# Kernel tuning notes

Hardware: AMD Instinct MI355X
Metric: run time of the kernel (lower is better)

The kernel has to match this reference:

```python
import jax, jax.numpy as jnp
import numpy as np

N_NODES = 50000  # 4 node types x 12500
N_PER = 12500
E = 600000
H = 128
IN_DIMS = [128, 128, 64, 64]


def setup_inputs() -> dict:
    key = jax.random.key(0)
    ks = jax.random.split(key, 16)
    inp = {}
    for i, d in enumerate(IN_DIMS):
        inp[f"feat{i}"] = jax.random.normal(ks[i], (N_PER, d), dtype=jnp.float32)
        # xavier_normal-ish init, gain 1.414
        std = 1.414 * np.sqrt(2.0 / (d + H))
        inp[f"W_fc{i}"] = jax.random.normal(ks[4 + i], (d, H), dtype=jnp.float32) * std
        inp[f"b_fc{i}"] = jnp.zeros((H,), dtype=jnp.float32)
    inp["src"] = jax.random.randint(ks[8], (E,), 0, N_NODES, dtype=jnp.int32)
    inp["dst"] = jax.random.randint(ks[9], (E,), 0, N_NODES, dtype=jnp.int32)
    inp["e_feat"] = jax.random.randint(ks[10], (E,), 0, 36, dtype=jnp.int32)
    inp["b_g0"] = jnp.zeros((H,), dtype=jnp.float32)  # GraphConv layer0 (weight=False, bias)
    inp["W_g1"] = jax.random.normal(ks[11], (H, H), dtype=jnp.float32) * np.sqrt(1.0 / H)
    inp["b_g1"] = jnp.zeros((H,), dtype=jnp.float32)
    return inp


def _degree_norms(src, dst):
    ones = jnp.ones((src.shape[0],), dtype=jnp.float32)
    deg_out = jax.ops.segment_sum(ones, src, num_segments=N_NODES)
    deg_in = jax.ops.segment_sum(ones, dst, num_segments=N_NODES)
    # DGL norm='both': D_out^{-1/2} on src side, D_in^{-1/2} on dst side (clamp 0-degree)
    out_norm = jax.lax.rsqrt(jnp.maximum(deg_out, 1.0))
    in_norm = jax.lax.rsqrt(jnp.maximum(deg_in, 1.0))
    return out_norm, in_norm


def _gcn_aggregate(h, src, dst, out_norm, in_norm):
    m = (h * out_norm[:, None])[src]                      # [E, H] gather
    agg = jax.ops.segment_sum(m, dst, num_segments=N_NODES)
    return agg * in_norm[:, None]


def reference(feat0, feat1, feat2, feat3,
              W_fc0, b_fc0, W_fc1, b_fc1, W_fc2, b_fc2, W_fc3, b_fc3,
              src, dst, e_feat, b_g0, W_g1, b_g1):
    # per-node-type linear projections, then concat along node dim
    h = jnp.concatenate([
        feat0 @ W_fc0 + b_fc0,
        feat1 @ W_fc1 + b_fc1,
        feat2 @ W_fc2 + b_fc2,
        feat3 @ W_fc3 + b_fc3,
    ], axis=0)  # [N_NODES, H]

    out_norm, in_norm = _degree_norms(src, dst)
    # GraphConv layer 0: weight=False, bias, activation (dropout p=0 -> identity)
    h = jax.nn.relu(_gcn_aggregate(h, src, dst, out_norm, in_norm) + b_g0)
    # GraphConv layer 1: aggregate, then linear weight + bias, activation
    h = jax.nn.relu(_gcn_aggregate(h, src, dst, out_norm, in_norm) @ W_g1 + b_g1)

    e = e_feat.astype(jnp.float32)  # e_feat.reshape(-1,1).float() in original
    # forward graph: msg = ft + sum_{r in 0..4} where(e==r, ft, 0) = ft * (1 + 1{e in 0..4})
    w_fwd = 1.0 + sum((e == float(r)).astype(jnp.float32) for r in (0, 1, 2, 3, 4))
    agg_a = jax.ops.segment_sum(h[src] * w_fwd[:, None], dst, num_segments=N_NODES)
    # transpose graph (reversed edges, same e): msg = sum_{r in {6,14,30}} where(e==r, ft, 0)
    w_bwd = sum((e == float(r)).astype(jnp.float32) for r in (6, 14, 30))
    agg_b = jax.ops.segment_sum(h[dst] * w_bwd[:, None], src, num_segments=N_NODES)
    return agg_a + agg_b
```

## Files before the change

### kernel.cpp

```cpp
#include <hip/hip_runtime.h>
#include <hip/hip_bf16.h>

#define N_NODES 50000
#define N_PER   12500
#define E_EDGES 600000
#define HDIM    128

#define NBLK_FC    ((N_PER + 63) / 64)
#define NBLK_NODE  ((N_NODES + 255) / 256)
#define MASK31  0x7fffffff

#define HQD 64
#define HSL_D (E_EDGES / HQD)
#define NBLK_DB (HQD * 4)

typedef __attribute__((ext_vector_type(8))) short bfrag;
typedef __attribute__((ext_vector_type(4))) float ffrag;

__device__ __forceinline__ unsigned short f2bf(float f) {
    union { float f; unsigned u; } x; x.f = f;
    unsigned r = x.u + 0x7fffu + ((x.u >> 16) & 1u);
    return (unsigned short)(r >> 16);
}
__device__ __forceinline__ float lo_bf(unsigned v) { return __uint_as_float(v << 16); }
__device__ __forceinline__ float hi_bf(unsigned v) { return __uint_as_float(v & 0xffff0000u); }
__device__ __forceinline__ unsigned pack2(float a, float b) {
    return (unsigned)f2bf(a) | ((unsigned)f2bf(b) << 16);
}
__device__ __forceinline__ float onrm_of(int deg) {
    return rsqrtf(fmaxf((float)deg, 1.0f));
}

__device__ __forceinline__ void acc8_add(float* acc, uint4 v) {
    acc[0] += lo_bf(v.x); acc[1] += hi_bf(v.x);
    acc[2] += lo_bf(v.y); acc[3] += hi_bf(v.y);
    acc[4] += lo_bf(v.z); acc[5] += hi_bf(v.z);
    acc[6] += lo_bf(v.w); acc[7] += hi_bf(v.w);
}
__device__ __forceinline__ void acc8_addw(float* acc, uint4 v, float w) {
    acc[0] += lo_bf(v.x) * w; acc[1] += hi_bf(v.x) * w;
    acc[2] += lo_bf(v.y) * w; acc[3] += hi_bf(v.y) * w;
    acc[4] += lo_bf(v.z) * w; acc[5] += hi_bf(v.z) * w;
    acc[6] += lo_bf(v.w) * w; acc[7] += hi_bf(v.w) * w;
}

__global__ __launch_bounds__(1024) void prep_kernel(
    const float* __restrict__ W0, const float* __restrict__ W1,
    const float* __restrict__ W2, const float* __restrict__ W3,
    const float* __restrict__ Wg,
    const int* __restrict__ src, const int* __restrict__ dst,
    const int* __restrict__ ef,
    unsigned short* __restrict__ Wp,
    unsigned* __restrict__ partial) {
    __shared__ unsigned hist[N_PER];
    int b = blockIdx.x;
    if (b < NBLK_DB) {
        const int q = b >> 2;
        const int p = b & 3;
        const int g0 = p * N_PER;
        for (int j = threadIdx.x; j < N_PER; j += 1024) hist[j] = 0;
        __syncthreads();
        const int e0 = q * HSL_D;
        for (int i = e0 + threadIdx.x; i < e0 + HSL_D; i += 1024) {
            int d = dst[i], t = ef[i], s = src[i];
            unsigned rd = (unsigned)(d - g0);
            if (rd < (unsigned)N_PER) atomicAdd(&hist[rd], 1u);
            unsigned rs = (unsigned)(s - g0);
            if (rs < (unsigned)N_PER) {
                unsigned inc = 0x10000u
                             + ((t == 6 || t == 14 || t == 30) ? 0x400u : 0u);
                atomicAdd(&hist[rs], inc);
            }
        }
        __syncthreads();
        for (int j = threadIdx.x; j < N_PER; j += 1024)
            partial[(size_t)q * N_NODES + g0 + j] = hist[j];
    } else {
        int tid = (b - NBLK_DB) * 1024 + threadIdx.x;
        const float* W; int D, base, off;
        if      (tid < 2048) { W = W0; D = 128; base = 0;    off = 0;     }
        else if (tid < 4096) { W = W1; D = 128; base = 2048; off = 16384; }
        else if (tid < 5120) { W = W2; D = 64;  base = 4096; off = 32768; }
        else if (tid < 6144) { W = W3; D = 64;  base = 5120; off = 40960; }
        else                 { W = Wg; D = 128; base = 6144; off = 49152; }
        int t2 = tid - base;
        int KT = D / 32;
        int l = t2 & 63;
        int tt = t2 >> 6;
        int kt = tt % KT, n0 = tt / KT;
        int n = n0 * 16 + (l & 15);
        int kb = kt * 32 + (l >> 4) * 8;
#pragma unroll
        for (int j = 0; j < 8; ++j)
            Wp[(size_t)off + (size_t)t2 * 8 + j] = f2bf(W[(size_t)(kb + j) * 128 + n]);
    }
}

__global__ __launch_bounds__(256) void plane_prefix_kernel(
    unsigned* __restrict__ partial,
    int* __restrict__ degD, int* __restrict__ degB,
    int* __restrict__ scanD, int* __restrict__ scanB,
    int* __restrict__ blocksumD, int* __restrict__ blocksumB,
    float* __restrict__ onrm_buf) {
    const int t = threadIdx.x;
    const int n = blockIdx.x * 256 + t;
    int dA = 0, dD = 0, dB = 0;
    if (n < N_NODES) {
        int runD = 0, runB = 0, dS = 0;
#pragma unroll
        for (int q = 0; q < HQD; ++q) {
            size_t ix = (size_t)q * N_NODES + n;
            unsigned w = partial[ix];
            partial[ix] = (unsigned)runD | ((unsigned)runB << 10);
            runD += (int)(w & 0x3FFu);
            runB += (int)((w >> 10) & 0x3Fu);
            dS   += (int)(w >> 16);
        }
        dD = runD; dB = runB;
        degD[n] = dD; degB[n] = dB;
        onrm_buf[n] = onrm_of(dS);
        dA = (dD + 3) & ~3;
    }
    __shared__ int sD[256], sB[256];
    sD[t] = dA; sB[t] = dB;
    __syncthreads();
    for (int off = 1; off < 256; off <<= 1) {
        int xD = (t >= off) ? sD[t - off] : 0;
        int xB = (t >= off) ? sB[t - off] : 0;
        __syncthreads();
        sD[t] += xD; sB[t] += xB;
        __syncthreads();
    }
    if (n < N_NODES) {
        scanD[n] = sD[t] - dA;
        scanB[n] = sB[t] - dB;
    }
    if (t == 255) {
        blocksumD[blockIdx.x] = sD[255];
        blocksumB[blockIdx.x] = sB[255];
    }
}

__global__ __launch_bounds__(256) void base_add_kernel(
    const int* __restrict__ blocksumD, const int* __restrict__ blocksumB,
    const int* __restrict__ scanD, const int* __restrict__ scanB,
    const int* __restrict__ degD, const int* __restrict__ degB,
    int2* __restrict__ csrD, int2* __restrict__ csrB) {
    __shared__ int sD[256], sB[256];
    const int t = threadIdx.x;
    const int bid = blockIdx.x;
    sD[t] = (t < bid) ? blocksumD[t] : 0;
    sB[t] = (t < bid) ? blocksumB[t] : 0;
    __syncthreads();
    for (int off = 128; off >= 1; off >>= 1) {
        if (t < off) { sD[t] += sD[t + off]; sB[t] += sB[t + off]; }
        __syncthreads();
    }
    const int n = bid * 256 + t;
    if (n < N_NODES) {
        csrD[n] = make_int2(scanD[n] + sD[0], degD[n]);
        csrB[n] = make_int2(scanB[n] + sB[0], degB[n]);
    }
}

template<int D>
__device__ __forceinline__ void fc_body(
    int blk, int tid,
    const float* __restrict__ X,
    const unsigned short* __restrict__ Wp,
    const float* __restrict__ bias,
    const float* __restrict__ onrm,
    unsigned short* __restrict__ outbf,
    int rows)
{
    constexpr int KT = D / 32;
    const int lane = tid & 63;
    const int wave = tid >> 6;
    const int m = lane & 15, q = lane >> 4;
    const int rbase = blk * 64 + wave * 16;
    const int row = rbase + m;

    bfrag afr[KT];
#pragma unroll
    for (int kt = 0; kt < KT; ++kt) {
        bfrag a;
        if (row < rows) {
            const float* xp = X + (size_t)row * D + kt * 32 + q * 8;
            float4 u0 = *(const float4*)xp;
            float4 u1 = *(const float4*)(xp + 4);
            a[0] = (short)f2bf(u0.x); a[1] = (short)f2bf(u0.y);
            a[2] = (short)f2bf(u0.z); a[3] = (short)f2bf(u0.w);
            a[4] = (short)f2bf(u1.x); a[5] = (short)f2bf(u1.y);
            a[6] = (short)f2bf(u1.z); a[7] = (short)f2bf(u1.w);
        } else {
#pragma unroll
            for (int t = 0; t < 8; ++t) a[t] = 0;
        }
        afr[kt] = a;
    }

    ffrag acc[8];
#pragma unroll
    for (int n0 = 0; n0 < 8; ++n0)
#pragma unroll
        for (int t = 0; t < 4; ++t) acc[n0][t] = 0.f;

#pragma unroll
    for (int n0 = 0; n0 < 8; ++n0)
#pragma unroll
        for (int kt = 0; kt < KT; ++kt) {
            bfrag bfr = *(const bfrag*)(Wp + ((size_t)(n0 * KT + kt) * 64 + lane) * 8);
            acc[n0] = __builtin_amdgcn_mfma_f32_16x16x32_bf16(afr[kt], bfr, acc[n0], 0, 0, 0);
        }

#pragma unroll
    for (int n0 = 0; n0 < 8; ++n0) {
        const int col = n0 * 16 + m;
        const float bj = bias[col];
#pragma unroll
        for (int r = 0; r < 4; ++r) {
            int orow = rbase + q * 4 + r;
            if (orow < rows)
                outbf[(size_t)orow * 128 + col] =
                    f2bf((acc[n0][r] + bj) * onrm[orow]);
        }
    }
}

__global__ __launch_bounds__(1024) void scatfc_kernel(
    const int* __restrict__ src, const int* __restrict__ dst,
    const int* __restrict__ ef,
    const unsigned* __restrict__ partial,
    const int2* __restrict__ csrD, const int2* __restrict__ csrB,
    int* __restrict__ bucket, int* __restrict__ bucketB,
    const float* __restrict__ f0, const float* __restrict__ f1,
    const float* __restrict__ f2, const float* __restrict__ f3,
    const unsigned short* __restrict__ Wp,
    const float* __restrict__ b0, const float* __restrict__ b1,
    const float* __restrict__ b2, const float* __restrict__ b3,
    const float* __restrict__ onrm_buf,
    unsigned short* __restrict__ Abf)
{
    __shared__ unsigned offP[N_PER];
    const int b = blockIdx.x;
    if (b < NBLK_DB) {
        const int q = b >> 2;
        const int p = b & 3;
        const int g0 = p * N_PER;
        for (int j = threadIdx.x; j < N_PER; j += 1024) {
            unsigned w = partial[(size_t)q * N_NODES + g0 + j];
            offP[j] = (unsigned)(csrD[g0 + j].x + (int)(w & 0x3FFu))
                    | (((w >> 10) & 0x3Fu) << 20);
        }
        __syncthreads();
        const int e0 = q * HSL_D;
        for (int i = e0 + threadIdx.x; i < e0 + HSL_D; i += 1024) {
            int s = src[i], d = dst[i], t = ef[i];
            unsigned rd = (unsigned)(d - g0);
            if (rd < (unsigned)N_PER) {
                unsigned old = atomicAdd(&offP[rd], 1u);
                bucket[old & 0xFFFFFu] = s | ((t <= 4) ? 0x80000000 : 0);
            }
            if (t == 6 || t == 14 || t == 30) {
                unsigned rs = (unsigned)(s - g0);
                if (rs < (unsigned)N_PER) {
                    unsigned old = atomicAdd(&offP[rs], 1u << 20);
                    bucketB[csrB[s].x + (int)(old >> 20)] = d;
                }
            }
        }
    } else {
        int ft = (b - NBLK_DB) * 4 + (threadIdx.x >> 8);
        int tid = threadIdx.x & 255;
        int which = ft / NBLK_FC;
        int blk = ft - which * NBLK_FC;
        if (which == 0)
            fc_body<128>(blk, tid, f0, Wp,         b0, onrm_buf,
                         Abf + (size_t)0 * N_PER * HDIM, N_PER);
        else if (which == 1)
            fc_body<128>(blk, tid, f1, Wp + 16384, b1, onrm_buf + N_PER,
                         Abf + (size_t)1 * N_PER * HDIM, N_PER);
        else if (which == 2)
            fc_body<64>(blk, tid, f2, Wp + 32768, b2, onrm_buf + 2 * N_PER,
                        Abf + (size_t)2 * N_PER * HDIM, N_PER);
        else
            fc_body<64>(blk, tid, f3, Wp + 40960, b3, onrm_buf + 3 * N_PER,
                        Abf + (size_t)3 * N_PER * HDIM, N_PER);
    }
}

#define GATHER8(DSTARR)                                                       \
    for (; i + 8 <= cnt; i += 8) {                                            \
        int4 c0 = *(const int4*)(bk + i);                                     \
        int4 c1 = *(const int4*)(bk + i + 4);                                 \
        int cc[8] = {c0.x, c0.y, c0.z, c0.w, c1.x, c1.y, c1.z, c1.w};         \
        uint4 v[8];                                                           \
        _Pragma("unroll")                                                     \
        for (int k = 0; k < 8; ++k)                                           \
            v[k] = DSTARR[(size_t)(cc[k] & MASK31) * 16 + j8];                \
        _Pragma("unroll")                                                     \
        for (int k = 0; k < 8; ++k) acc8_add(acc, v[k]);                      \
    }                                                                         \
    if (i + 4 <= cnt) {                                                       \
        int4 c0 = *(const int4*)(bk + i);                                     \
        int cc[4] = {c0.x, c0.y, c0.z, c0.w};                                 \
        uint4 v[4];                                                           \
        _Pragma("unroll")                                                     \
        for (int k = 0; k < 4; ++k)                                           \
            v[k] = DSTARR[(size_t)(cc[k] & MASK31) * 16 + j8];                \
        _Pragma("unroll")                                                     \
        for (int k = 0; k < 4; ++k) acc8_add(acc, v[k]);                      \
        i += 4;                                                               \
    }                                                                         \
    for (; i < cnt; ++i)                                                      \
        acc8_add(acc, DSTARR[(size_t)(bk[i] & MASK31) * 16 + j8]);

__global__ __launch_bounds__(256) void agg0g_kernel(
    const uint4* __restrict__ A,
    const int* __restrict__ bucket, const int2* __restrict__ csrD,
    const float* __restrict__ onrm_buf, const float* __restrict__ b_g0,
    const unsigned short* __restrict__ Wp,
    unsigned short* __restrict__ BW) {
    __shared__ uint4 Bt[256];
    const int tdx = threadIdx.x;
    const int nloc = tdx >> 4, j8 = tdx & 15;
    const int n = blockIdx.x * 16 + nloc;

    const int2 cd = csrD[n];
    const int cnt = cd.y;
    const int* bk = bucket + cd.x;
    float acc[8] = {0.f, 0.f, 0.f, 0.f, 0.f, 0.f, 0.f, 0.f};
    int i = 0;
    GATHER8(A)

    float inr = onrm_of(cnt);
    float onr = onrm_buf[n];
    const float* bg = b_g0 + j8 * 8;
    float r[8];
#pragma unroll
    for (int k = 0; k < 8; ++k)
        r[k] = fmaxf(acc[k] * inr + bg[k], 0.f) * onr;
    uint4 o;
    o.x = pack2(r[0], r[1]); o.y = pack2(r[2], r[3]);
    o.z = pack2(r[4], r[5]); o.w = pack2(r[6], r[7]);
    Bt[j8 * 16 + nloc] = o;
    __syncthreads();

    const int lane = tdx & 63;
    const int wave = tdx >> 6;
    const int m = lane & 15, q = lane >> 4;

    bfrag afr[4];
#pragma unroll
    for (int kt = 0; kt < 4; ++kt)
        afr[kt] = *(const bfrag*)(Bt + (kt * 4 + q) * 16 + m);

    ffrag acc2[2];
#pragma unroll
    for (int t2 = 0; t2 < 2; ++t2) {
#pragma unroll
        for (int t = 0; t < 4; ++t) acc2[t2][t] = 0.f;
        const int n0 = wave * 2 + t2;
#pragma unroll
        for (int kt = 0; kt < 4; ++kt) {
            bfrag bfr = *(const bfrag*)(Wp + ((size_t)(n0 * 4 + kt) * 64 + lane) * 8);
            acc2[t2] = __builtin_amdgcn_mfma_f32_16x16x32_bf16(afr[kt], bfr, acc2[t2], 0, 0, 0);
        }
    }

    const int rowbase = blockIdx.x * 16;
#pragma unroll
    for (int t2 = 0; t2 < 2; ++t2) {
        const int col = (wave * 2 + t2) * 16 + m;
#pragma unroll
        for (int rr = 0; rr < 4; ++rr) {
            const int row = rowbase + q * 4 + rr;
            BW[(size_t)row * 128 + col] = f2bf(acc2[t2][rr]);
        }
    }
}

__global__ __launch_bounds__(256) void agg1_kernel(
    const uint4* __restrict__ BW,
    const int* __restrict__ bucket, const int2* __restrict__ csrD,
    const float* __restrict__ b_g1,
    uint4* __restrict__ H) {
    int idx = blockIdx.x * blockDim.x + threadIdx.x;
    int n = idx >> 4, j8 = idx & 15;
    const int2 cd = csrD[n];
    const int cnt = cd.y;
    const int* bk = bucket + cd.x;
    float acc[8] = {0.f, 0.f, 0.f, 0.f, 0.f, 0.f, 0.f, 0.f};
    int i = 0;
    GATHER8(BW)
    float inr = onrm_of(cnt);
    const float* bg = b_g1 + j8 * 8;
    float r[8];
#pragma unroll
    for (int k = 0; k < 8; ++k)
        r[k] = fmaxf(acc[k] * inr + bg[k], 0.f);
    uint4 o;
    o.x = pack2(r[0], r[1]); o.y = pack2(r[2], r[3]);
    o.z = pack2(r[4], r[5]); o.w = pack2(r[6], r[7]);
    H[(size_t)n * 16 + j8] = o;
}

__global__ __launch_bounds__(256) void final_kernel(
    const uint4* __restrict__ H,
    const int* __restrict__ bucket, const int2* __restrict__ csrD,
    const int* __restrict__ bucketB, const int2* __restrict__ csrB,
    float4* __restrict__ out4) {
    int idx = blockIdx.x * blockDim.x + threadIdx.x;
    int n = idx >> 4, j8 = idx & 15;
    float acc[8] = {0.f, 0.f, 0.f, 0.f, 0.f, 0.f, 0.f, 0.f};
    const int2 cd = csrD[n];
    const int cnt = cd.y;
    const int* bk = bucket + cd.x;
    int i = 0;
    for (; i + 8 <= cnt; i += 8) {
        int4 c0 = *(const int4*)(bk + i);
        int4 c1 = *(const int4*)(bk + i + 4);
        int cc[8] = {c0.x, c0.y, c0.z, c0.w, c1.x, c1.y, c1.z, c1.w};
        uint4 v[8];
#pragma unroll
        for (int k = 0; k < 8; ++k)
            v[k] = H[(size_t)(cc[k] & MASK31) * 16 + j8];
#pragma unroll
        for (int k = 0; k < 8; ++k)
            acc8_addw(acc, v[k], (cc[k] < 0) ? 2.0f : 1.0f);
    }
    if (i + 4 <= cnt) {
        int4 c0 = *(const int4*)(bk + i);
        int cc[4] = {c0.x, c0.y, c0.z, c0.w};
        uint4 v[4];
#pragma unroll
        for (int k = 0; k < 4; ++k)
            v[k] = H[(size_t)(cc[k] & MASK31) * 16 + j8];
#pragma unroll
        for (int k = 0; k < 4; ++k)
            acc8_addw(acc, v[k], (cc[k] < 0) ? 2.0f : 1.0f);
        i += 4;
    }
    for (; i < cnt; ++i) {
        int c = bk[i];
        acc8_addw(acc, H[(size_t)(c & MASK31) * 16 + j8], (c < 0) ? 2.0f : 1.0f);
    }
    const int2 cb = csrB[n];
    const int* bkB = bucketB + cb.x;
    for (int k = 0; k < cb.y; ++k)
        acc8_add(acc, H[(size_t)bkB[k] * 16 + j8]);
    float4 o0 = {acc[0], acc[1], acc[2], acc[3]};
    float4 o1 = {acc[4], acc[5], acc[6], acc[7]};
    out4[(size_t)n * 32 + j8 * 2]     = o0;
    out4[(size_t)n * 32 + j8 * 2 + 1] = o1;
}

extern "C" void kernel_launch(void* const* d_in, const int* in_sizes, int n_in,
                              void* d_out, int out_size, void* d_ws, size_t ws_size,
                              hipStream_t stream) {
    const float* feat[4]  = {(const float*)d_in[0], (const float*)d_in[3],
                             (const float*)d_in[6], (const float*)d_in[9]};
    const float* W_fc[4]  = {(const float*)d_in[1], (const float*)d_in[4],
                             (const float*)d_in[7], (const float*)d_in[10]};
    const float* b_fc[4]  = {(const float*)d_in[2], (const float*)d_in[5],
                             (const float*)d_in[8], (const float*)d_in[11]};
    const int*   src      = (const int*)d_in[12];
    const int*   dst      = (const int*)d_in[13];
    const int*   efeat    = (const int*)d_in[14];
    const float* b_g0     = (const float*)d_in[15];
    const float* W_g1     = (const float*)d_in[16];
    const float* b_g1     = (const float*)d_in[17];
    float* out = (float*)d_out;

    char* p = (char*)d_ws;
    unsigned short* Abf = (unsigned short*)p; p += (size_t)N_NODES * HDIM * 2;
    unsigned short* Bbf = (unsigned short*)p; p += (size_t)N_NODES * HDIM * 2;
    unsigned short* Wp  = (unsigned short*)p; p += (size_t)65536 * 2;
    int* bucket  = (int*)p; p += (size_t)(E_EDGES + 4 * N_NODES) * 4;
    int* bucketB = (int*)p; p += (size_t)E_EDGES * 4;
    unsigned* partial = (unsigned*)p; p += (size_t)HQD * N_NODES * 4;
    int* degD  = (int*)p; p += (size_t)N_NODES * 4;
    int* degB  = (int*)p; p += (size_t)N_NODES * 4;
    int* scanD = (int*)p; p += (size_t)N_NODES * 4;
    int* scanB = (int*)p; p += (size_t)N_NODES * 4;
    int2* csrD = (int2*)p; p += (size_t)N_NODES * 8;
    int2* csrB = (int2*)p; p += (size_t)N_NODES * 8;
    float* onrm_buf = (float*)p; p += (size_t)N_NODES * 4;
    int* blocksumD = (int*)p; p += 256 * 4;
    int* blocksumB = (int*)p; p += 256 * 4;

    const unsigned short* Wpg = Wp + 49152;

    prep_kernel<<<NBLK_DB + 8, 1024, 0, stream>>>(
        W_fc[0], W_fc[1], W_fc[2], W_fc[3], W_g1, src, dst, efeat,
        Wp, partial);

    plane_prefix_kernel<<<NBLK_NODE, 256, 0, stream>>>(
        partial, degD, degB, scanD, scanB, blocksumD, blocksumB, onrm_buf);

    base_add_kernel<<<NBLK_NODE, 256, 0, stream>>>(
        blocksumD, blocksumB, scanD, scanB, degD, degB, csrD, csrB);

    scatfc_kernel<<<NBLK_DB + NBLK_FC, 1024, 0, stream>>>(
        src, dst, efeat, partial, csrD, csrB, bucket, bucketB,
        feat[0], feat[1], feat[2], feat[3], Wp,
        b_fc[0], b_fc[1], b_fc[2], b_fc[3], onrm_buf, Abf);

    const int grid_node = (N_NODES * 16) / 256;

    agg0g_kernel<<<grid_node, 256, 0, stream>>>(
        (const uint4*)Abf, bucket, csrD, onrm_buf, b_g0, Wpg, Bbf);

    agg1_kernel<<<grid_node, 256, 0, stream>>>(
        (const uint4*)Bbf, bucket, csrD, b_g1, (uint4*)Abf);

    final_kernel<<<grid_node, 256, 0, stream>>>(
        (const uint4*)Abf, bucket, csrD, bucketB, csrB, (float4*)out);
}
```

Baseline: 226.2 us.

## Sort nodes by in-degree into a permutation to balance aggregation waves

Builds a degree histogram (bins 0..63) per block during the prefix pass, then computes a global counting-sort permutation of nodes by in-degree in the base-add kernel. The three aggregation kernels iterate over nodes through this permutation, so nodes with similar edge counts share a wave and divergence from uneven loop trip counts shrinks. The cost is an extra indirection per node, scattered output writes instead of contiguous ones, and some extra histogram work in the setup kernels. Reads from the feature array may also lose some locality.

```diff
diff --git a/kernel.cpp b/kernel.cpp
--- a/kernel.cpp
+++ b/kernel.cpp
@@ -101,9 +101,14 @@
     int* __restrict__ degD, int* __restrict__ degB,
     int* __restrict__ scanD, int* __restrict__ scanB,
     int* __restrict__ blocksumD, int* __restrict__ blocksumB,
-    float* __restrict__ onrm_buf) {
+    float* __restrict__ onrm_buf,
+    int* __restrict__ binpartT) {
+    __shared__ int sD[256], sB[256];
+    __shared__ unsigned binh[64];
     const int t = threadIdx.x;
     const int n = blockIdx.x * 256 + t;
+    if (t < 64) binh[t] = 0;
+    __syncthreads();
     int dA = 0, dD = 0, dB = 0;
     if (n < N_NODES) {
         int runD = 0, runB = 0, dS = 0;
@@ -120,8 +125,8 @@
         degD[n] = dD; degB[n] = dB;
         onrm_buf[n] = onrm_of(dS);
         dA = (dD + 3) & ~3;
-    }
-    __shared__ int sD[256], sB[256];
+        atomicAdd(&binh[min(dD, 63)], 1u);
+    }
     sD[t] = dA; sB[t] = dB;
     __syncthreads();
     for (int off = 1; off < 256; off <<= 1) {
@@ -139,14 +144,20 @@
         blocksumD[blockIdx.x] = sD[255];
         blocksumB[blockIdx.x] = sB[255];
     }
+    if (t < 64)
+        binpartT[t * NBLK_NODE + blockIdx.x] = (int)binh[t];
 }
 
 __global__ __launch_bounds__(256) void base_add_kernel(
     const int* __restrict__ blocksumD, const int* __restrict__ blocksumB,
     const int* __restrict__ scanD, const int* __restrict__ scanB,
     const int* __restrict__ degD, const int* __restrict__ degB,
-    int2* __restrict__ csrD, int2* __restrict__ csrB) {
+    const int* __restrict__ binpartT,
+    int2* __restrict__ csrD, int2* __restrict__ csrB,
+    int* __restrict__ perm) {
     __shared__ int sD[256], sB[256];
+    __shared__ int binfull[64], binpart_[64], binbase[64];
+    __shared__ unsigned binh[64];
     const int t = threadIdx.x;
     const int bid = blockIdx.x;
     sD[t] = (t < bid) ? blocksumD[t] : 0;
@@ -156,10 +167,37 @@
         if (t < off) { sD[t] += sD[t + off]; sB[t] += sB[t + off]; }
         __syncthreads();
     }
+    if (t < 64) {
+        binh[t] = 0;
+        int cf = 0, cp = 0;
+        const int4* bp = (const int4*)(binpartT + t * NBLK_NODE);
+#pragma unroll 8
+        for (int j4 = 0; j4 < 49; ++j4) {
+            int4 v = bp[j4];
+            int bj = j4 * 4;
+            cf += v.x + v.y + v.z + v.w;
+            cp += ((bj     < bid) ? v.x : 0) + ((bj + 1 < bid) ? v.y : 0)
+                + ((bj + 2 < bid) ? v.z : 0) + ((bj + 3 < bid) ? v.w : 0);
+        }
+        binfull[t] = cf; binpart_[t] = cp;
+    }
+    __syncthreads();
+    if (t == 0) {
+        int run = 0;
+        for (int bb = 0; bb < 64; ++bb) {
+            int c = binfull[bb]; binfull[bb] = run; run += c;
+        }
+    }
+    __syncthreads();
+    if (t < 64) binbase[t] = binfull[t] + binpart_[t];
+    __syncthreads();
     const int n = bid * 256 + t;
     if (n < N_NODES) {
         csrD[n] = make_int2(scanD[n] + sD[0], degD[n]);
         csrB[n] = make_int2(scanB[n] + sB[0], degB[n]);
+        int bin = min(degD[n], 63);
+        unsigned rank = atomicAdd(&binh[bin], 1u);
+        perm[binbase[bin] + (int)rank] = n;
     }
 }
 
@@ -320,11 +358,14 @@
     const int* __restrict__ bucket, const int2* __restrict__ csrD,
     const float* __restrict__ onrm_buf, const float* __restrict__ b_g0,
     const unsigned short* __restrict__ Wp,
+    const int* __restrict__ perm,
     unsigned short* __restrict__ BW) {
     __shared__ uint4 Bt[256];
+    __shared__ int pnode[16];
     const int tdx = threadIdx.x;
     const int nloc = tdx >> 4, j8 = tdx & 15;
-    const int n = blockIdx.x * 16 + nloc;
+    const int n = perm[blockIdx.x * 16 + nloc];
+    if (tdx < 16) pnode[tdx] = perm[blockIdx.x * 16 + tdx];
 
     const int2 cd = csrD[n];
     const int cnt = cd.y;
@@ -368,13 +409,12 @@
         }
     }
 
-    const int rowbase = blockIdx.x * 16;
 #pragma unroll
     for (int t2 = 0; t2 < 2; ++t2) {
         const int col = (wave * 2 + t2) * 16 + m;
 #pragma unroll
         for (int rr = 0; rr < 4; ++rr) {
-            const int row = rowbase + q * 4 + rr;
+            const int row = pnode[q * 4 + rr];
             BW[(size_t)row * 128 + col] = f2bf(acc2[t2][rr]);
         }
     }
@@ -384,9 +424,11 @@
     const uint4* __restrict__ BW,
     const int* __restrict__ bucket, const int2* __restrict__ csrD,
     const float* __restrict__ b_g1,
+    const int* __restrict__ perm,
     uint4* __restrict__ H) {
     int idx = blockIdx.x * blockDim.x + threadIdx.x;
-    int n = idx >> 4, j8 = idx & 15;
+    int n = perm[idx >> 4];
+    int j8 = idx & 15;
     const int2 cd = csrD[n];
     const int cnt = cd.y;
     const int* bk = bucket + cd.x;
@@ -409,9 +451,11 @@
     const uint4* __restrict__ H,
     const int* __restrict__ bucket, const int2* __restrict__ csrD,
     const int* __restrict__ bucketB, const int2* __restrict__ csrB,
+    const int* __restrict__ perm,
     float4* __restrict__ out4) {
     int idx = blockIdx.x * blockDim.x + threadIdx.x;
-    int n = idx >> 4, j8 = idx & 15;
+    int n = perm[idx >> 4];
+    int j8 = idx & 15;
     float acc[8] = {0.f, 0.f, 0.f, 0.f, 0.f, 0.f, 0.f, 0.f};
     const int2 cd = csrD[n];
     const int cnt = cd.y;
@@ -488,6 +532,8 @@
     float* onrm_buf = (float*)p; p += (size_t)N_NODES * 4;
     int* blocksumD = (int*)p; p += 256 * 4;
     int* blocksumB = (int*)p; p += 256 * 4;
+    int* binpartT  = (int*)p; p += (size_t)64 * NBLK_NODE * 4;
+    int* perm      = (int*)p; p += (size_t)N_NODES * 4;
 
     const unsigned short* Wpg = Wp + 49152;
 
@@ -496,10 +542,12 @@
         Wp, partial);
 
     plane_prefix_kernel<<<NBLK_NODE, 256, 0, stream>>>(
-        partial, degD, degB, scanD, scanB, blocksumD, blocksumB, onrm_buf);
+        partial, degD, degB, scanD, scanB, blocksumD, blocksumB, onrm_buf,
+        binpartT);
 
     base_add_kernel<<<NBLK_NODE, 256, 0, stream>>>(
-        blocksumD, blocksumB, scanD, scanB, degD, degB, csrD, csrB);
+        blocksumD, blocksumB, scanD, scanB, degD, degB, binpartT,
+        csrD, csrB, perm);
 
     scatfc_kernel<<<NBLK_DB + NBLK_FC, 1024, 0, stream>>>(
         src, dst, efeat, partial, csrD, csrB, bucket, bucketB,
@@ -509,11 +557,11 @@
     const int grid_node = (N_NODES * 16) / 256;
 
     agg0g_kernel<<<grid_node, 256, 0, stream>>>(
-        (const uint4*)Abf, bucket, csrD, onrm_buf, b_g0, Wpg, Bbf);
+        (const uint4*)Abf, bucket, csrD, onrm_buf, b_g0, Wpg, perm, Bbf);
 
     agg1_kernel<<<grid_node, 256, 0, stream>>>(
-        (const uint4*)Bbf, bucket, csrD, b_g1, (uint4*)Abf);
+        (const uint4*)Bbf, bucket, csrD, b_g1, perm, (uint4*)Abf);
 
     final_kernel<<<grid_node, 256, 0, stream>>>(
-        (const uint4*)Abf, bucket, csrD, bucketB, csrB, (float4*)out);
-}
+        (const uint4*)Abf, bucket, csrD, bucketB, csrB, perm, (float4*)out);
+}
```

After: 236.2 us. 4.4% more time.
